# Optimization experiments

Hardware: AMD Instinct MI355X
Metric: run time of the kernel (lower is better)

Reference implementation:

```python
import jax, jax.numpy as jnp
import numpy as np

B, S, I, H, F1, C = 1024, 512, 50, 64, 32, 2


def setup_inputs() -> dict:
    key = jax.random.key(0)
    ks = jax.random.split(key, 9)
    s_ih = 1.0 / np.sqrt(H)
    return {
        "x": jax.random.normal(ks[0], (B, S, I), dtype=jnp.float32),
        # PyTorch LSTM params, gate order (i, f, g, o) stacked along dim 0
        "W_ih": jax.random.uniform(ks[1], (4 * H, I), jnp.float32, -s_ih, s_ih),
        "W_hh": jax.random.uniform(ks[2], (4 * H, H), jnp.float32, -s_ih, s_ih),
        "b_ih": jax.random.uniform(ks[3], (4 * H,), jnp.float32, -s_ih, s_ih),
        "b_hh": jax.random.uniform(ks[4], (4 * H,), jnp.float32, -s_ih, s_ih),
        "W1": jax.random.uniform(ks[5], (F1, H), jnp.float32, -s_ih, s_ih),
        "b1": jax.random.uniform(ks[6], (F1,), jnp.float32, -s_ih, s_ih),
        "W2": jax.random.uniform(ks[7], (C, F1), jnp.float32, -1.0 / np.sqrt(F1), 1.0 / np.sqrt(F1)),
        "b2": jax.random.uniform(ks[8], (C,), jnp.float32, -1.0 / np.sqrt(F1), 1.0 / np.sqrt(F1)),
    }


def _lstm_last(x, W_ih, W_hh, b_ih, b_hh):
    # Precompute input contribution for all timesteps in one big GEMM: [B,S,4H]
    xg = jnp.einsum("bsi,gi->bsg", x, W_ih) + b_ih + b_hh
    Bn = x.shape[0]
    Hn = W_hh.shape[1]
    h0 = jnp.zeros((Bn, Hn), dtype=x.dtype)
    c0 = jnp.zeros((Bn, Hn), dtype=x.dtype)

    def step(carry, xt):
        h, c = carry
        g = xt + h @ W_hh.T  # [B,4H]
        i_g, f_g, g_g, o_g = jnp.split(g, 4, axis=-1)
        i_g = jax.nn.sigmoid(i_g)
        f_g = jax.nn.sigmoid(f_g)
        g_g = jnp.tanh(g_g)
        o_g = jax.nn.sigmoid(o_g)
        c_new = f_g * c + i_g * g_g
        h_new = o_g * jnp.tanh(c_new)
        return (h_new, c_new), None

    (h_last, _), _ = jax.lax.scan(step, (h0, c0), xg.transpose(1, 0, 2))
    return h_last  # == out[:, -1, :]


def reference(x, W_ih, W_hh, b_ih, b_hh, W1, b1, W2, b2):
    last_out = _lstm_last(x, W_ih, W_hh, b_ih, b_hh)
    # Dropout is identity in eval mode (deterministic reference)
    h = jax.nn.relu(last_out @ W1.T + b1)
    return h @ W2.T + b2  # [B, num_classes]
```

## Files before the change

kernel.cpp:

```cpp
#include <hip/hip_runtime.h>
#include <math.h>


#define S_LEN  512
#define I_DIM  50
#define H_DIM  64
#define BB     4
#define TC     16
#define NCH    (S_LEN / TC)
#define KROW   40
#define XROW   72
#define XSHALF (BB * TC * XROW)
#define NXE    (BB * TC * I_DIM)
#define F1_DIM 32
#define C_DIM  2
#define ILO    (1.0f / 2048.0f)

typedef __attribute__((ext_vector_type(8))) _Float16 f16x8;
typedef __attribute__((ext_vector_type(4))) float    f32x4;

__device__ __forceinline__ float fast_rcp(float x) { return __builtin_amdgcn_rcpf(x); }
__device__ __forceinline__ float sigm(float v) { return fast_rcp(1.0f + __expf(-v)); }
__device__ __forceinline__ float tanh_fast(float v) {
    return 1.0f - 2.0f * fast_rcp(__expf(2.0f * v) + 1.0f);
}

__device__ __forceinline__ void load_wfrag(const float* __restrict__ Wih,
                                           const float* __restrict__ Whh,
                                           int ktg, int row, int hk,
                                           f16x8& bh, f16x8& bl) {
    #pragma unroll
    for (int j = 0; j < 8; ++j) {
        const int kk = ktg * 32 + hk * 8 + j;
        float wv;
        if (ktg < 2) wv = (kk < I_DIM) ? Wih[row * I_DIM + kk] : 0.0f;
        else         wv = Whh[row * H_DIM + (kk - 64)];
        const _Float16 h = (_Float16)wv;
        bh[j] = h;
        bl[j] = (_Float16)((wv - (float)h) * 2048.0f);
    }
}

#define MFMA16(A, B, C) __builtin_amdgcn_mfma_f32_16x16x32_f16(A, B, C, 0, 0, 0)

#define BAR() do { asm volatile("s_waitcnt lgkmcnt(0)" ::: "memory"); \
                   __builtin_amdgcn_s_barrier(); } while (0)

__global__ __launch_bounds__(512, 1)
void lstm_mfma(const float* __restrict__ x,
               const float* __restrict__ W_ih, const float* __restrict__ W_hh,
               const float* __restrict__ b_ih, const float* __restrict__ b_hh,
               const float* __restrict__ W1,  const float* __restrict__ b1,
               const float* __restrict__ W2,  const float* __restrict__ b2,
               float* __restrict__ out)
{
    __shared__ __align__(16) _Float16 Hst[2][2][16][KROW];
    __shared__ __align__(16) _Float16 Xs[2][BB * TC][XROW];
    __shared__ __align__(16) float    XGb[2][TC][BB][H_DIM][4];
    __shared__ float f1buf[BB][F1_DIM];

    const int u  = threadIdx.x;
    const int w  = u >> 6;
    const int l  = u & 63;
    const int c  = l & 15;
    const int hk = l >> 4;
    const int b0 = blockIdx.x * BB;
    const bool is_scan = (w < 4);
    const int q  = w & 3;
    const f32x4 Z4 = {0.f, 0.f, 0.f, 0.f};

    f16x8 s00h, s00l, s01h, s01l, s10h, s10l, s11h, s11l,
          s20h, s20l, s21h, s21l, s30h, s30l, s31h, s31l;
    f16x8 g00h, g00l, g01h, g01l, g10h, g10l, g11h, g11l,
          g20h, g20l, g21h, g21l, g30h, g30l, g31h, g31l;
    float bs0 = 0.f, bs1 = 0.f, bs2 = 0.f, bs3 = 0.f;
    float cst = 0.0f;

    f16x8 ga0, ga1;
    f32x4 G0, H0, G1, H1, G2, H2, G3, H3;

    const float *xp0=x,*xp1=x,*xp2=x,*xp3=x,*xp4=x,*xp5=x,*xp6=x,
                *xp7=x,*xp8=x,*xp9=x,*xp10=x,*xp11=x,*xp12=x;
    int  ld0=0,ld1=0,ld2=0,ld3=0,ld4=0,ld5=0,ld6=0,ld7=0,ld8=0,ld9=0,ld10=0,ld11=0,ld12=0;
    bool v0=false,v1=false,v2=false,v3=false,v4=false,v5=false,v6=false,
         v7=false,v8=false,v9=false,v10=false,v11=false,v12=false;

    if (is_scan) {
        const int base = 16 * w + c;
        load_wfrag(W_ih, W_hh, 2, 0 * H_DIM + base, hk, s00h, s00l);
        load_wfrag(W_ih, W_hh, 3, 0 * H_DIM + base, hk, s01h, s01l);
        load_wfrag(W_ih, W_hh, 2, 1 * H_DIM + base, hk, s10h, s10l);
        load_wfrag(W_ih, W_hh, 3, 1 * H_DIM + base, hk, s11h, s11l);
        load_wfrag(W_ih, W_hh, 2, 2 * H_DIM + base, hk, s20h, s20l);
        load_wfrag(W_ih, W_hh, 3, 2 * H_DIM + base, hk, s21h, s21l);
        load_wfrag(W_ih, W_hh, 2, 3 * H_DIM + base, hk, s30h, s30l);
        load_wfrag(W_ih, W_hh, 3, 3 * H_DIM + base, hk, s31h, s31l);
    } else {
        const int base = 16 * q + c;
        load_wfrag(W_ih, W_hh, 0, 0 * H_DIM + base, hk, g00h, g00l);
        load_wfrag(W_ih, W_hh, 1, 0 * H_DIM + base, hk, g01h, g01l);
        load_wfrag(W_ih, W_hh, 0, 1 * H_DIM + base, hk, g10h, g10l);
        load_wfrag(W_ih, W_hh, 1, 1 * H_DIM + base, hk, g11h, g11l);
        load_wfrag(W_ih, W_hh, 0, 2 * H_DIM + base, hk, g20h, g20l);
        load_wfrag(W_ih, W_hh, 1, 2 * H_DIM + base, hk, g21h, g21l);
        load_wfrag(W_ih, W_hh, 0, 3 * H_DIM + base, hk, g30h, g30l);
        load_wfrag(W_ih, W_hh, 1, 3 * H_DIM + base, hk, g31h, g31l);
        bs0 = b_ih[0 * H_DIM + base] + b_hh[0 * H_DIM + base];
        bs1 = b_ih[1 * H_DIM + base] + b_hh[1 * H_DIM + base];
        bs2 = b_ih[2 * H_DIM + base] + b_hh[2 * H_DIM + base];
        bs3 = b_ih[3 * H_DIM + base] + b_hh[3 * H_DIM + base];

        const int ug = u - 256;
#define PRE(E) { const int idx = ug + (E) * 256; if (idx < NXE) { \
            const int bb_ = idx / (TC * I_DIM); \
            const int rm_ = idx - bb_ * (TC * I_DIM); \
            const int t_  = rm_ / I_DIM; \
            const int ii_ = rm_ - t_ * I_DIM; \
            xp##E = x + (size_t)(b0 + bb_) * (S_LEN * I_DIM) + t_ * I_DIM + ii_; \
            ld##E = (bb_ * TC + t_) * XROW + ii_; v##E = true; } }
        PRE(0) PRE(1) PRE(2) PRE(3) PRE(4) PRE(5) PRE(6)
        PRE(7) PRE(8) PRE(9) PRE(10) PRE(11) PRE(12)
#undef PRE
    }

    for (int i = u; i < 1280; i += 512) ((unsigned*)Hst)[i] = 0u;
    for (int i = u; i < 4608; i += 512) ((unsigned*)Xs)[i]  = 0u;
    __syncthreads();

    if (!is_scan) {
#define STG(E, CH, BUF) if (v##E) { \
        const float t_ = xp##E[(size_t)(CH) * (TC * I_DIM)]; \
        *((_Float16*)Xs + (BUF) * XSHALF + ld##E) = (_Float16)t_; }
        STG(0,0,0) STG(1,0,0) STG(2,0,0) STG(3,0,0) STG(4,0,0) STG(5,0,0)
        STG(6,0,0) STG(7,0,0) STG(8,0,0) STG(9,0,0) STG(10,0,0) STG(11,0,0) STG(12,0,0)
        STG(0,1,1) STG(1,1,1) STG(2,1,1) STG(3,1,1) STG(4,1,1) STG(5,1,1)
        STG(6,1,1) STG(7,1,1) STG(8,1,1) STG(9,1,1) STG(10,1,1) STG(11,1,1) STG(12,1,1)
#undef STG
    }
    __syncthreads();

#define GPK(DB, MT, I) { f32x4 pk; \
    pk[0] = G0[I] + fmaf(ILO, H0[I], bs0); \
    pk[1] = G1[I] + fmaf(ILO, H1[I], bs1); \
    pk[2] = G2[I] + fmaf(ILO, H2[I], bs2); \
    pk[3] = G3[I] + fmaf(ILO, H3[I], bs3); \
    *(f32x4*)&XGb[DB][4 * hk + (I)][MT][16 * q + c][0] = pk; }

#define GQ0(SB, MT) { \
    ga0 = *(const f16x8*)&Xs[SB][(MT) * 16 + c][hk * 8]; \
    ga1 = *(const f16x8*)&Xs[SB][(MT) * 16 + c][32 + hk * 8]; \
    G0 = MFMA16(ga0, g00h, Z4); G0 = MFMA16(ga1, g01h, G0); \
    H0 = MFMA16(ga0, g00l, Z4); H0 = MFMA16(ga1, g01l, H0); }
#define GQ1() { \
    G1 = MFMA16(ga0, g10h, Z4); G1 = MFMA16(ga1, g11h, G1); \
    H1 = MFMA16(ga0, g10l, Z4); H1 = MFMA16(ga1, g11l, H1); }
#define GQ2() { \
    G2 = MFMA16(ga0, g20h, Z4); G2 = MFMA16(ga1, g21h, G2); \
    H2 = MFMA16(ga0, g20l, Z4); H2 = MFMA16(ga1, g21l, H2); }
#define GQ3(DB, MT) { \
    G3 = MFMA16(ga0, g30h, Z4); G3 = MFMA16(ga1, g31h, G3); \
    H3 = MFMA16(ga0, g30l, Z4); H3 = MFMA16(ga1, g31l, H3); \
    GPK(DB, MT, 0) GPK(DB, MT, 1) GPK(DB, MT, 2) GPK(DB, MT, 3) }

    if (!is_scan) {
        GQ0(0, 0) GQ1() GQ2() GQ3(0, 0)
        GQ0(0, 1) GQ1() GQ2() GQ3(0, 1)
        GQ0(0, 2) GQ1() GQ2() GQ3(0, 2)
        GQ0(0, 3) GQ1() GQ2() GQ3(0, 3)
    }
    __syncthreads();

#define SCAN_STEP(TT, CUR) { \
    const int p = (TT) & 1; \
    const f16x8 ah0 = *(const f16x8*)&Hst[p][0][c][hk * 8]; \
    const f16x8 ah1 = *(const f16x8*)&Hst[p][1][c][hk * 8]; \
    const f32x4 xg4 = *(const f32x4*)&XGb[CUR][TT][hk][16 * w + c][0]; \
    __builtin_amdgcn_s_setprio(1); \
    f32x4 A0 = MFMA16(ah0, s00h, Z4); A0 = MFMA16(ah1, s01h, A0); \
    f32x4 L0 = MFMA16(ah0, s00l, Z4); L0 = MFMA16(ah1, s01l, L0); \
    f32x4 A1 = MFMA16(ah0, s10h, Z4); A1 = MFMA16(ah1, s11h, A1); \
    f32x4 L1 = MFMA16(ah0, s10l, Z4); L1 = MFMA16(ah1, s11l, L1); \
    f32x4 A2 = MFMA16(ah0, s20h, Z4); A2 = MFMA16(ah1, s21h, A2); \
    f32x4 L2 = MFMA16(ah0, s20l, Z4); L2 = MFMA16(ah1, s21l, L2); \
    f32x4 A3 = MFMA16(ah0, s30h, Z4); A3 = MFMA16(ah1, s31h, A3); \
    f32x4 L3 = MFMA16(ah0, s30l, Z4); L3 = MFMA16(ah1, s31l, L3); \
    __builtin_amdgcn_s_setprio(0); \
    const float p0 = A0[0] + fmaf(ILO, L0[0], xg4[0]); \
    const float p1 = A1[0] + fmaf(ILO, L1[0], xg4[1]); \
    const float p2 = A2[0] + fmaf(ILO, L2[0], xg4[2]); \
    const float p3 = A3[0] + fmaf(ILO, L3[0], xg4[3]); \
    const float gi = sigm(p0), gf = sigm(p1); \
    const float gg = tanh_fast(p2), go = sigm(p3); \
    cst = fmaf(gf, cst, gi * gg); \
    const float hv = go * tanh_fast(cst); \
    const int uo = 16 * w + c; \
    Hst[p ^ 1][uo >> 5][4 * hk][uo & 31] = (_Float16)hv; }

#define XISS(E, CH2) if (v##E) xr##E = xp##E[(size_t)(CH2) * (TC * I_DIM)];
#define XCMT(E, BUF) if (v##E) *((_Float16*)Xs + (BUF) * XSHALF + ld##E) = (_Float16)xr##E;

    for (int ch = 0; ch < NCH; ++ch) {
        const int cur = ch & 1, nx = cur ^ 1;
        const bool cmp = (ch + 1 < NCH);
        const bool stg = (ch + 2 < NCH);
        float xr0=0,xr1=0,xr2=0,xr3=0,xr4=0,xr5=0,xr6=0,
              xr7=0,xr8=0,xr9=0,xr10=0,xr11=0,xr12=0;

        #pragma unroll
        for (int tt = 0; tt < TC; ++tt) {
            if (is_scan) {
                SCAN_STEP(tt, cur)
            } else {
                if (cmp) {
                    const int mt = tt >> 2, gq = tt & 3;
                    if (gq == 0) { GQ0(nx, mt) }
                    if (gq == 1) { GQ1() }
                    if (gq == 2) { GQ2() }
                    if (gq == 3) { GQ3(nx, mt) }
                }
                if (stg) {
                    if (tt == 0) {
                        XISS(0, ch+2) XISS(1, ch+2) XISS(2, ch+2) XISS(3, ch+2)
                        XISS(4, ch+2) XISS(5, ch+2) XISS(6, ch+2) XISS(7, ch+2)
                        XISS(8, ch+2) XISS(9, ch+2) XISS(10, ch+2) XISS(11, ch+2)
                        XISS(12, ch+2)
                    }
                    if (tt == 6)  { XCMT(0, cur)  XCMT(1, cur) }
                    if (tt == 7)  { XCMT(2, cur)  XCMT(3, cur) }
                    if (tt == 8)  { XCMT(4, cur)  XCMT(5, cur) }
                    if (tt == 9)  { XCMT(6, cur)  XCMT(7, cur) }
                    if (tt == 10) { XCMT(8, cur)  XCMT(9, cur) }
                    if (tt == 11) { XCMT(10, cur) XCMT(11, cur) }
                    if (tt == 12) { XCMT(12, cur) }
                }
            }
            BAR();
        }
    }
#undef SCAN_STEP
#undef GQ0
#undef GQ1
#undef GQ2
#undef GQ3
#undef GPK
#undef XISS
#undef XCMT

    __syncthreads();

    if (u < BB * F1_DIM) {
        const int b = u >> 5, f = u & 31;
        float acc = b1[f];
        #pragma unroll
        for (int j = 0; j < H_DIM; ++j) {
            const float hj = (float)Hst[0][j >> 5][4 * b][j & 31];
            acc = fmaf(hj, W1[f * H_DIM + j], acc);
        }
        f1buf[b][f] = fmaxf(acc, 0.0f);
    }
    __syncthreads();
    if (u < BB * C_DIM) {
        const int b = u >> 1, cl = u & 1;
        float acc = b2[cl];
        #pragma unroll
        for (int f = 0; f < F1_DIM; ++f)
            acc = fmaf(f1buf[b][f], W2[cl * F1_DIM + f], acc);
        out[(size_t)(b0 + b) * C_DIM + cl] = acc;
    }
}

extern "C" void kernel_launch(void* const* d_in, const int* in_sizes, int n_in,
                              void* d_out, int out_size, void* d_ws, size_t ws_size,
                              hipStream_t stream) {
    const float* x   = (const float*)d_in[0];
    const float* Wih = (const float*)d_in[1];
    const float* Whh = (const float*)d_in[2];
    const float* bih = (const float*)d_in[3];
    const float* bhh = (const float*)d_in[4];
    const float* W1  = (const float*)d_in[5];
    const float* b1  = (const float*)d_in[6];
    const float* W2  = (const float*)d_in[7];
    const float* b2  = (const float*)d_in[8];
    float* out = (float*)d_out;

    hipLaunchKernelGGL(lstm_mfma, dim3(256), dim3(512), 0, stream,
                       x, Wih, Whh, bih, bhh, W1, b1, W2, b2, out);
}
```

Before: 204.2 us.

## Split recurrent scan across eight waves with two gates per lane and shuffles

The recurrent scan moves from four waves to eight. Each lane now computes two gate pre-activations (i/g or f/o) instead of all four, and pairs of lanes exchange values with __shfl_xor so that half the lanes apply the cell update. This halves the MFMA chain per wave on the serial critical path, at the cost of a larger block (768 threads), extra shuffles, and idle lanes during the elementwise phase. The input-GEMM waves are shifted to wave indices 8-11.

```diff
diff --git a/kernel.cpp b/kernel.cpp
--- a/kernel.cpp
+++ b/kernel.cpp
@@ -46,7 +46,7 @@
 #define BAR() do { asm volatile("s_waitcnt lgkmcnt(0)" ::: "memory"); \
                    __builtin_amdgcn_s_barrier(); } while (0)
 
-__global__ __launch_bounds__(512, 1)
+__global__ __launch_bounds__(768, 3)
 void lstm_mfma(const float* __restrict__ x,
                const float* __restrict__ W_ih, const float* __restrict__ W_hh,
                const float* __restrict__ b_ih, const float* __restrict__ b_hh,
@@ -65,12 +65,14 @@
     const int c  = l & 15;
     const int hk = l >> 4;
     const int b0 = blockIdx.x * BB;
-    const bool is_scan = (w < 4);
+    const bool is_scan = (w < 8);
     const int q  = w & 3;
     const f32x4 Z4 = {0.f, 0.f, 0.f, 0.f};
 
-    f16x8 s00h, s00l, s01h, s01l, s10h, s10l, s11h, s11l,
-          s20h, s20l, s21h, s21l, s30h, s30l, s31h, s31l;
+    const int un = 8 * (w & 7) + (c & 7);
+    const int gh = c >> 3;
+
+    f16x8 sA0h, sA0l, sA1h, sA1l, sB0h, sB0l, sB1h, sB1l;
     f16x8 g00h, g00l, g01h, g01l, g10h, g10l, g11h, g11l,
           g20h, g20l, g21h, g21l, g30h, g30l, g31h, g31l;
     float bs0 = 0.f, bs1 = 0.f, bs2 = 0.f, bs3 = 0.f;
@@ -82,19 +84,14 @@
     const float *xp0=x,*xp1=x,*xp2=x,*xp3=x,*xp4=x,*xp5=x,*xp6=x,
                 *xp7=x,*xp8=x,*xp9=x,*xp10=x,*xp11=x,*xp12=x;
     int  ld0=0,ld1=0,ld2=0,ld3=0,ld4=0,ld5=0,ld6=0,ld7=0,ld8=0,ld9=0,ld10=0,ld11=0,ld12=0;
-    bool v0=false,v1=false,v2=false,v3=false,v4=false,v5=false,v6=false,
-         v7=false,v8=false,v9=false,v10=false,v11=false,v12=false;
+    bool v0_=false,v1_=false,v2_=false,v3_=false,v4_=false,v5_=false,v6_=false,
+         v7_=false,v8_=false,v9_=false,v10_=false,v11_=false,v12_=false;
 
     if (is_scan) {
-        const int base = 16 * w + c;
-        load_wfrag(W_ih, W_hh, 2, 0 * H_DIM + base, hk, s00h, s00l);
-        load_wfrag(W_ih, W_hh, 3, 0 * H_DIM + base, hk, s01h, s01l);
-        load_wfrag(W_ih, W_hh, 2, 1 * H_DIM + base, hk, s10h, s10l);
-        load_wfrag(W_ih, W_hh, 3, 1 * H_DIM + base, hk, s11h, s11l);
-        load_wfrag(W_ih, W_hh, 2, 2 * H_DIM + base, hk, s20h, s20l);
-        load_wfrag(W_ih, W_hh, 3, 2 * H_DIM + base, hk, s21h, s21l);
-        load_wfrag(W_ih, W_hh, 2, 3 * H_DIM + base, hk, s30h, s30l);
-        load_wfrag(W_ih, W_hh, 3, 3 * H_DIM + base, hk, s31h, s31l);
+        load_wfrag(W_ih, W_hh, 2, gh * H_DIM + un,       hk, sA0h, sA0l);
+        load_wfrag(W_ih, W_hh, 3, gh * H_DIM + un,       hk, sA1h, sA1l);
+        load_wfrag(W_ih, W_hh, 2, (gh + 2) * H_DIM + un, hk, sB0h, sB0l);
+        load_wfrag(W_ih, W_hh, 3, (gh + 2) * H_DIM + un, hk, sB1h, sB1l);
     } else {
         const int base = 16 * q + c;
         load_wfrag(W_ih, W_hh, 0, 0 * H_DIM + base, hk, g00h, g00l);
@@ -110,25 +107,25 @@
         bs2 = b_ih[2 * H_DIM + base] + b_hh[2 * H_DIM + base];
         bs3 = b_ih[3 * H_DIM + base] + b_hh[3 * H_DIM + base];
 
-        const int ug = u - 256;
+        const int ug = u - 512;
 #define PRE(E) { const int idx = ug + (E) * 256; if (idx < NXE) { \
             const int bb_ = idx / (TC * I_DIM); \
             const int rm_ = idx - bb_ * (TC * I_DIM); \
             const int t_  = rm_ / I_DIM; \
             const int ii_ = rm_ - t_ * I_DIM; \
             xp##E = x + (size_t)(b0 + bb_) * (S_LEN * I_DIM) + t_ * I_DIM + ii_; \
-            ld##E = (bb_ * TC + t_) * XROW + ii_; v##E = true; } }
+            ld##E = (bb_ * TC + t_) * XROW + ii_; v##E##_ = true; } }
         PRE(0) PRE(1) PRE(2) PRE(3) PRE(4) PRE(5) PRE(6)
         PRE(7) PRE(8) PRE(9) PRE(10) PRE(11) PRE(12)
 #undef PRE
     }
 
-    for (int i = u; i < 1280; i += 512) ((unsigned*)Hst)[i] = 0u;
-    for (int i = u; i < 4608; i += 512) ((unsigned*)Xs)[i]  = 0u;
+    for (int i = u; i < 1280; i += 768) ((unsigned*)Hst)[i] = 0u;
+    for (int i = u; i < 4608; i += 768) ((unsigned*)Xs)[i]  = 0u;
     __syncthreads();
 
     if (!is_scan) {
-#define STG(E, CH, BUF) if (v##E) { \
+#define STG(E, CH, BUF) if (v##E##_) { \
         const float t_ = xp##E[(size_t)(CH) * (TC * I_DIM)]; \
         *((_Float16*)Xs + (BUF) * XSHALF + ld##E) = (_Float16)t_; }
         STG(0,0,0) STG(1,0,0) STG(2,0,0) STG(3,0,0) STG(4,0,0) STG(5,0,0)
@@ -174,30 +171,28 @@
     const int p = (TT) & 1; \
     const f16x8 ah0 = *(const f16x8*)&Hst[p][0][c][hk * 8]; \
     const f16x8 ah1 = *(const f16x8*)&Hst[p][1][c][hk * 8]; \
-    const f32x4 xg4 = *(const f32x4*)&XGb[CUR][TT][hk][16 * w + c][0]; \
+    const float xgA = XGb[CUR][TT][hk][un][gh]; \
+    const float xgB = XGb[CUR][TT][hk][un][gh + 2]; \
     __builtin_amdgcn_s_setprio(1); \
-    f32x4 A0 = MFMA16(ah0, s00h, Z4); A0 = MFMA16(ah1, s01h, A0); \
-    f32x4 L0 = MFMA16(ah0, s00l, Z4); L0 = MFMA16(ah1, s01l, L0); \
-    f32x4 A1 = MFMA16(ah0, s10h, Z4); A1 = MFMA16(ah1, s11h, A1); \
-    f32x4 L1 = MFMA16(ah0, s10l, Z4); L1 = MFMA16(ah1, s11l, L1); \
-    f32x4 A2 = MFMA16(ah0, s20h, Z4); A2 = MFMA16(ah1, s21h, A2); \
-    f32x4 L2 = MFMA16(ah0, s20l, Z4); L2 = MFMA16(ah1, s21l, L2); \
-    f32x4 A3 = MFMA16(ah0, s30h, Z4); A3 = MFMA16(ah1, s31h, A3); \
-    f32x4 L3 = MFMA16(ah0, s30l, Z4); L3 = MFMA16(ah1, s31l, L3); \
+    f32x4 A0 = MFMA16(ah0, sA0h, Z4); A0 = MFMA16(ah1, sA1h, A0); \
+    f32x4 L0 = MFMA16(ah0, sA0l, Z4); L0 = MFMA16(ah1, sA1l, L0); \
+    f32x4 B0 = MFMA16(ah0, sB0h, Z4); B0 = MFMA16(ah1, sB1h, B0); \
+    f32x4 L1 = MFMA16(ah0, sB0l, Z4); L1 = MFMA16(ah1, sB1l, L1); \
     __builtin_amdgcn_s_setprio(0); \
-    const float p0 = A0[0] + fmaf(ILO, L0[0], xg4[0]); \
-    const float p1 = A1[0] + fmaf(ILO, L1[0], xg4[1]); \
-    const float p2 = A2[0] + fmaf(ILO, L2[0], xg4[2]); \
-    const float p3 = A3[0] + fmaf(ILO, L3[0], xg4[3]); \
-    const float gi = sigm(p0), gf = sigm(p1); \
-    const float gg = tanh_fast(p2), go = sigm(p3); \
-    cst = fmaf(gf, cst, gi * gg); \
-    const float hv = go * tanh_fast(cst); \
-    const int uo = 16 * w + c; \
-    Hst[p ^ 1][uo >> 5][4 * hk][uo & 31] = (_Float16)hv; }
-
-#define XISS(E, CH2) if (v##E) xr##E = xp##E[(size_t)(CH2) * (TC * I_DIM)];
-#define XCMT(E, BUF) if (v##E) *((_Float16*)Xs + (BUF) * XSHALF + ld##E) = (_Float16)xr##E;
+    const float v0 = A0[0] + fmaf(ILO, L0[0], xgA);    \
+    const float v1 = B0[0] + fmaf(ILO, L1[0], xgB);    \
+    const float y0 = __shfl_xor(v0, 8); \
+    const float y1 = __shfl_xor(v1, 8); \
+    if (c < 8) { \
+        const float gi = sigm(v0), gf = sigm(y0); \
+        const float gg = tanh_fast(v1), go = sigm(y1); \
+        cst = fmaf(gf, cst, gi * gg); \
+        const float hv = go * tanh_fast(cst); \
+        Hst[p ^ 1][un >> 5][4 * hk][un & 31] = (_Float16)hv; \
+    } }
+
+#define XISS(E, CH2) if (v##E##_) xr##E = xp##E[(size_t)(CH2) * (TC * I_DIM)];
+#define XCMT(E, BUF) if (v##E##_) *((_Float16*)Xs + (BUF) * XSHALF + ld##E) = (_Float16)xr##E;
 
     for (int ch = 0; ch < NCH; ++ch) {
         const int cur = ch & 1, nx = cur ^ 1;
@@ -283,6 +278,6 @@
     const float* b2  = (const float*)d_in[8];
     float* out = (float*)d_out;
 
-    hipLaunchKernelGGL(lstm_mfma, dim3(256), dim3(512), 0, stream,
+    hipLaunchKernelGGL(lstm_mfma, dim3(256), dim3(768), 0, stream,
                        x, Wih, Whh, bih, bhh, W1, b1, W2, b2, out);
 }
```

New measurement: 299.1 us. +46.4%, slower.
